# Performance work log

Hardware: AMD Instinct MI355X
Metric: run time of the kernel (lower is better)

Reference implementation:

```python
import jax, jax.numpy as jnp
import numpy as np


def _hat(w):
    # w [...,3] -> skew-symmetric [...,3,3]
    x, y, z = w[..., 0], w[..., 1], w[..., 2]
    o = jnp.zeros_like(x)
    return jnp.stack([
        jnp.stack([o, -z, y], -1),
        jnp.stack([z, o, -x], -1),
        jnp.stack([-y, x, o], -1)], -2)


def _expmap(twist):
    # SE(3) exponential map. twist [...,6] = (v, w); returns [...,4,4]
    v, w = twist[..., :3], twist[..., 3:]
    th = jnp.linalg.norm(w, axis=-1, keepdims=True)[..., None]  # [...,1,1]
    Wh = _hat(w)
    W2 = Wh @ Wh
    small = th < 1e-4
    safe = jnp.where(small, 1.0, th)
    A = jnp.where(small, 1.0 - th * th / 6.0, jnp.sin(safe) / safe)
    Bc = jnp.where(small, 0.5 - th * th / 24.0, (1.0 - jnp.cos(safe)) / (safe * safe))
    Cc = jnp.where(small, 1.0 / 6.0 - th * th / 120.0, (safe - jnp.sin(safe)) / (safe ** 3))
    I = jnp.eye(3, dtype=twist.dtype)
    R = I + A * Wh + Bc * W2
    V = I + Bc * Wh + Cc * W2
    t = (V @ v[..., None])[..., 0]
    top = jnp.concatenate([R, t[..., None]], -1)  # [...,3,4]
    bot = jnp.broadcast_to(jnp.array([0.0, 0.0, 0.0, 1.0], twist.dtype), top.shape[:-2] + (1, 4))
    return jnp.concatenate([top, bot], -2)


def setup_inputs() -> dict:
    key = jax.random.key(0)
    ks = jax.random.split(key, 5)
    B, C, H, W = 2, 16, 32, 32
    embeddings = 0.3 * jax.random.normal(ks[0], (B, C, H, W), jnp.float32)
    revisions = 0.1 * jax.random.normal(ks[1], (B, 3, H, W), jnp.float32)
    weights = jax.random.uniform(ks[2], (B, 3, H, W), jnp.float32, 0.1, 1.0)
    depth = jax.random.uniform(ks[3], (B, 1, H, W), jnp.float32, 1.0, 5.0)
    pix = (jnp.zeros((4, 4), jnp.float32)
           .at[0, 0].set(float(W)).at[1, 1].set(float(W))
           .at[0, 2].set(W / 2.0).at[1, 2].set(H / 2.0)
           .at[2, 2].set(1.0).at[3, 3].set(1.0))
    pix_T_camXs = jnp.tile(pix[None], (B, 1, 1))
    twists = 0.02 * jax.random.normal(ks[4], (B, H, W, 6), jnp.float32)
    Tmat = _expmap(twists)  # valid SE(3) per pixel [B,H,W,4,4]
    return dict(embeddings=embeddings, revisions=revisions, weights=weights,
                depth=depth, pix_T_camXs=pix_T_camXs, Tmat=Tmat)


def reference(embeddings, revisions, weights, depth, pix_T_camXs, Tmat):
    B, C, H, W = embeddings.shape
    N = H * W
    dt = embeddings.dtype

    # pairwise embedding affinity exp(-||e_i - e_k||_2)  [B,N,N]
    e = embeddings.reshape(B, C, N).transpose(0, 2, 1)  # [B,N,C]
    diff = e[:, :, None, :] - e[:, None, :, :]
    aff = jnp.exp(-jnp.linalg.norm(diff, axis=-1))

    fx, fy = pix_T_camXs[:, 0, 0], pix_T_camXs[:, 1, 1]
    x0, y0 = pix_T_camXs[:, 0, 2], pix_T_camXs[:, 1, 2]

    # depth -> pointcloud [B,N,3]
    ys, xs = jnp.meshgrid(jnp.arange(H, dtype=dt), jnp.arange(W, dtype=dt), indexing='ij')
    u, v = xs.reshape(-1), ys.reshape(-1)
    z = depth.reshape(B, N)
    X = (u[None] - x0[:, None]) * z / fx[:, None]
    Y = (v[None] - y0[:, None]) * z / fy[:, None]
    xyz = jnp.stack([X, Y, z], -1)

    T = Tmat.reshape(B, N, 4, 4)
    Rm, tv = T[..., :3, :3], T[..., :3, 3]
    # T_k applied to its own point, and T_i (anchor) applied to every point
    TjXj = jnp.einsum('bkpq,bkq->bkp', Rm, xyz) + tv                    # [B,N,3]
    TiXj = jnp.einsum('bipq,bkq->bikp', Rm, xyz) + tv[:, :, None, :]     # [B,Ni,Nk,3]

    def pie(P):
        # projection (u, v, 1/Z)
        sh = (B,) + (1,) * (P.ndim - 2)
        invz = 1.0 / P[..., 2]
        uu = fx.reshape(sh) * P[..., 0] * invz + x0.reshape(sh)
        vv = fy.reshape(sh) * P[..., 1] * invz + y0.reshape(sh)
        return jnp.stack([uu, vv, invz], -1)

    pie_TjXj = pie(TjXj)   # [B,N,3]
    pie_TiXj = pie(TiXj)   # [B,Ni,Nk,3]

    r = revisions.reshape(B, 3, N).transpose(0, 2, 1)                   # [B,N,3]
    residual = pie_TiXj - (pie_TjXj + r)[:, None]                       # [B,Ni,Nk,3]

    # projection Jacobian wrt 3D point, d = 1/Z of transformed point
    d = pie_TiXj[..., 2]
    Xp, Yp = TiXj[..., 0], TiXj[..., 1]
    sh = (B, 1, 1)
    fxr, fyr = fx.reshape(sh), fy.reshape(sh)
    z0 = jnp.zeros_like(d)
    Jp = jnp.stack([
        jnp.stack([fxr * d, z0, -fxr * Xp * d * d], -1),
        jnp.stack([z0, fyr * d, -fyr * Yp * d * d], -1),
        jnp.stack([z0, z0, -d * d], -1)], -2)                            # [B,Ni,Nk,3,3]

    # transformation Jacobian [I | hat(X)]  [B,Nk,3,6]
    I3 = jnp.broadcast_to(jnp.eye(3, dtype=dt), (B, N, 3, 3))
    JT = jnp.concatenate([I3, _hat(xyz)], -1)

    Jac = jnp.einsum('bikpq,bkqr->bikpr', Jp, JT)                        # [B,Ni,Nk,3,6]

    wflat = weights.reshape(B, 3, N).transpose(0, 2, 1)                  # [B,Nk,3]
    wts = aff[..., None] * wflat[:, None]                                # [B,Ni,Nk,3]

    WJ = wts[..., None] * Jac
    Hm = jnp.einsum('bikcp,bikcq->bipq', WJ, Jac)                        # [B,Ni,6,6]
    rhs = jnp.einsum('bikcp,bikc->bip', Jac, residual)                   # [B,Ni,6]

    delta = jnp.einsum('bipq,biq->bip', jnp.linalg.inv(Hm), rhs)         # [B,N,6]

    dT = _expmap(delta.reshape(B, H, W, 6))                              # [B,H,W,4,4]
    return dT @ Tmat
```

## Files before the change

kernel.cpp:

```cpp
#include <hip/hip_runtime.h>
#include <math.h>

#define BB 2
#define CC 16
#define HH 32
#define WW 32
#define NN (HH*WW)
#define NPX (BB*NN)
#define PH  512

__global__ __launch_bounds__(512, 2)
void dse3_mono3(const float* __restrict__ emb,
                const float* __restrict__ rev,
                const float* __restrict__ wgt,
                const float* __restrict__ dep,
                const float* __restrict__ pix,
                const float* __restrict__ Tm,
                float* __restrict__ out)
{
    __shared__ float4 sE0[PH], sE1[PH], sE2[PH], sE3[PH], sQ0[PH], sQ1[PH];
    __shared__ float2 sQ2[PH];

    int tid  = threadIdx.x;
    int lane = tid & 63;
    int wv   = tid >> 6;
    int px   = blockIdx.x * 8 + wv;
    int b    = px >> 10;
    int kpx  = px & (NN - 1);

    float fx = pix[b*16 + 0], fy = pix[b*16 + 5];
    float x0 = pix[b*16 + 2], y0 = pix[b*16 + 6];
    float ifx = __builtin_amdgcn_rcpf(fx);
    float ify = __builtin_amdgcn_rcpf(fy);

    float ei[16];
    float sei = 0.f;
    #pragma unroll
    for (int c = 0; c < 16; ++c) {
        ei[c] = emb[(size_t)b*CC*NN + (size_t)c*NN + kpx];
        sei += ei[c]*ei[c];
    }
    const float4* Tp4 = (const float4*)(Tm + (size_t)px * 16);
    float4 Tr0 = Tp4[0], Tr1 = Tp4[1], Tr2 = Tp4[2];

    float aM0=0.f, aM2=0.f, aM4=0.f, aM5=0.f, aM8=0.f;
    float aN0=0.f, aN1=0.f, aN2=0.f, aN3=0.f, aN4=0.f,
          aN5=0.f, aN6=0.f, aN7=0.f, aN8=0.f;
    float aP0=0.f, aP1=0.f, aP2=0.f, aP3=0.f, aP4=0.f, aP5=0.f;
    float aR0=0.f, aR1=0.f, aR2=0.f, aR3=0.f, aR4=0.f, aR5=0.f;

    #pragma unroll
    for (int phase = 0; phase < 2; ++phase) {
        {
            int r  = tid;
            int k  = phase*PH + r;
            int gk = b*NN + k;

            float se = 0.f;
            float ev[16];
            #pragma unroll
            for (int c = 0; c < 16; ++c) {
                ev[c] = emb[(size_t)b*CC*NN + (size_t)c*NN + k];
                se += ev[c]*ev[c];
            }
            float u = (float)(k & (WW - 1));
            float v = (float)((k & (NN-1)) >> 5);
            float z = dep[b*NN + k];
            float X = (u - x0) * z * ifx;
            float Y = (v - y0) * z * ify;

            const float4* T4 = (const float4*)(Tm + (size_t)gk * 16);
            float4 t0 = T4[0], t1 = T4[1], t2 = T4[2];
            float Tx = t0.x*X + t0.y*Y + t0.z*z + t0.w;
            float Ty = t1.x*X + t1.y*Y + t1.z*z + t1.w;
            float Tz = t2.x*X + t2.y*Y + t2.z*z + t2.w;
            float di = __builtin_amdgcn_rcpf(Tz);

            float p0 = fx*Tx*di + x0 + rev[(size_t)b*3*NN + 0*NN + k];
            float p1 = fy*Ty*di + y0 + rev[(size_t)b*3*NN + 1*NN + k];
            float p2 = di            + rev[(size_t)b*3*NN + 2*NN + k];
            float w0 = wgt[(size_t)b*3*NN + 0*NN + k];
            float w1 = wgt[(size_t)b*3*NN + 1*NN + k];
            float w2 = wgt[(size_t)b*3*NN + 2*NN + k];

            sE0[r] = make_float4(ev[0],  ev[1],  ev[2],  ev[3]);
            sE1[r] = make_float4(ev[4],  ev[5],  ev[6],  ev[7]);
            sE2[r] = make_float4(ev[8],  ev[9],  ev[10], ev[11]);
            sE3[r] = make_float4(ev[12], ev[13], ev[14], ev[15]);
            sQ0[r] = make_float4(X, Y, z, p0);
            sQ1[r] = make_float4(p1, p2, w0, w1);
            sQ2[r] = make_float2(w2, se);
        }
        __syncthreads();

        #pragma unroll 2
        for (int j = 0; j < 8; ++j) {
            int r = j*64 + lane;

            float4 k0 = sE0[r], k1 = sE1[r], k2 = sE2[r], k3 = sE3[r];
            float4 q0 = sQ0[r], q1 = sQ1[r];
            float2 q2 = sQ2[r];

            float d0 = k0.x*ei[0]  + k0.y*ei[1]  + k0.z*ei[2]  + k0.w*ei[3];
            float d1 = k1.x*ei[4]  + k1.y*ei[5]  + k1.z*ei[6]  + k1.w*ei[7];
            float d2 = k2.x*ei[8]  + k2.y*ei[9]  + k2.z*ei[10] + k2.w*ei[11];
            float d3 = k3.x*ei[12] + k3.y*ei[13] + k3.z*ei[14] + k3.w*ei[15];
            float dot = (d0 + d1) + (d2 + d3);
            float ssq = fmaxf(sei + q2.y - 2.f*dot, 0.f);
            float aff = __expf(-__builtin_amdgcn_sqrtf(ssq));

            float X = q0.x, Y = q0.y, Z = q0.z;
            float Tx = Tr0.x*X + Tr0.y*Y + Tr0.z*Z + Tr0.w;
            float Ty = Tr1.x*X + Tr1.y*Y + Tr1.z*Z + Tr1.w;
            float Tz = Tr2.x*X + Tr2.y*Y + Tr2.z*Z + Tr2.w;
            float di = __builtin_amdgcn_rcpf(Tz);

            float a =  fx*di;
            float e =  fy*di;
            float uu = a*Tx;
            float vv = e*Ty;
            float r0 = uu + x0 - q0.w;
            float r1 = vv + y0 - q1.x;
            float r2 = di      - q1.y;
            float c = -uu*di;
            float f = -vv*di;
            float g = -di*di;

            float y0v = a*r0;
            float y1v = e*r1;
            float y2v = c*r0 + f*r1 + g*r2;
            aR0 += y0v; aR1 += y1v; aR2 += y2v;
            aR3 += Z*y1v - Y*y2v;
            aR4 += X*y2v - Z*y0v;
            aR5 += Y*y0v - X*y1v;

            float w0 = aff*q1.z, w1 = aff*q1.w, w2 = aff*q2.x;
            float aw = w0*a, ew = w1*e;
            float m00 = aw*a, m02 = aw*c;
            float m11 = ew*e, m12 = ew*f;
            float m22 = w0*c*c + w1*f*f + w2*g*g;
            aM0 += m00; aM2 += m02; aM4 += m11; aM5 += m12; aM8 += m22;

            float n00 = -m02*Y;
            float n01 =  m02*X - m00*Z;
            float n02 =  m00*Y;
            float n10 =  m11*Z - m12*Y;
            float n11 =  m12*X;
            float n12 = -m11*X;
            float n20 =  m12*Z - m22*Y;
            float n21 =  m22*X - m02*Z;
            float n22 =  m02*Y - m12*X;
            aN0 += n00; aN1 += n01; aN2 += n02;
            aN3 += n10; aN4 += n11; aN5 += n12;
            aN6 += n20; aN7 += n21; aN8 += n22;

            aP0 += Z*n10 - Y*n20;
            aP1 += Z*n11 - Y*n21;
            aP2 += Z*n12 - Y*n22;
            aP3 += X*n21 - Z*n01;
            aP4 += X*n22 - Z*n02;
            aP5 += Y*n02 - X*n12;
        }
        __syncthreads();
    }

    float acc[26] = { aM0,aM2,aM4,aM5,aM8,
                      aN0,aN1,aN2,aN3,aN4,aN5,aN6,aN7,aN8,
                      aP0,aP1,aP2,aP3,aP4,aP5,
                      aR0,aR1,aR2,aR3,aR4,aR5 };
    #pragma unroll
    for (int off = 32; off > 0; off >>= 1)
        #pragma unroll
        for (int t = 0; t < 26; ++t)
            acc[t] += __shfl_xor(acc[t], off, 64);

    if (lane != 0) return;

    float am[6][6];
    am[0][0]=acc[0]; am[0][1]=0.f;    am[0][2]=acc[1];
    am[1][1]=acc[2]; am[1][2]=acc[3]; am[2][2]=acc[4];
    am[0][3]=acc[5];  am[0][4]=acc[6];  am[0][5]=acc[7];
    am[1][3]=acc[8];  am[1][4]=acc[9];  am[1][5]=acc[10];
    am[2][3]=acc[11]; am[2][4]=acc[12]; am[2][5]=acc[13];
    am[3][3]=acc[14]; am[3][4]=acc[15]; am[3][5]=acc[16];
    am[4][4]=acc[17]; am[4][5]=acc[18]; am[5][5]=acc[19];
    #pragma unroll
    for (int p = 0; p < 6; ++p)
        #pragma unroll
        for (int q = 0; q < p; ++q) am[p][q] = am[q][p];
    float rh[6] = { acc[20], acc[21], acc[22], acc[23], acc[24], acc[25] };

    float L[6][6], dinv[6];
    #pragma unroll
    for (int p = 0; p < 6; ++p) {
        #pragma unroll
        for (int q = 0; q <= p; ++q) {
            float sm = am[p][q];
            #pragma unroll
            for (int r = 0; r < q; ++r) sm -= L[p][r]*L[q][r];
            if (q == p) {
                float sq = __builtin_amdgcn_sqrtf(sm);
                L[p][p] = sq;
                dinv[p] = __builtin_amdgcn_rcpf(sq);
            } else {
                L[p][q] = sm * dinv[q];
            }
        }
    }
    float yv[6];
    #pragma unroll
    for (int p = 0; p < 6; ++p) {
        float sm = rh[p];
        #pragma unroll
        for (int r = 0; r < p; ++r) sm -= L[p][r]*yv[r];
        yv[p] = sm * dinv[p];
    }
    float sol[6];
    #pragma unroll
    for (int pi = 5; pi >= 0; --pi) {
        float sm = yv[pi];
        #pragma unroll
        for (int r = pi + 1; r < 6; ++r) sm -= L[r][pi]*sol[r];
        sol[pi] = sm * dinv[pi];
    }

    float vx = sol[0], vy = sol[1], vz = sol[2];
    float wx = sol[3], wy = sol[4], wz = sol[5];
    float th2 = wx*wx + wy*wy + wz*wz;
    float th  = __builtin_amdgcn_sqrtf(th2);
    float Ae, Be, Ce;
    if (th < 1e-4f) {
        Ae = 1.0f - th2*(1.0f/6.0f);
        Be = 0.5f - th2*(1.0f/24.0f);
        Ce = 1.0f/6.0f - th2*(1.0f/120.0f);
    } else {
        float sn = __sinf(th), cn = __cosf(th);
        float ith = __builtin_amdgcn_rcpf(th), ith2 = ith*ith;
        Ae = sn*ith;
        Be = (1.0f - cn)*ith2;
        Ce = (th - sn)*ith2*ith;
    }
    float Wh[3][3] = {{0.f,-wz, wy},{ wz,0.f,-wx},{-wy, wx,0.f}};
    float W2[3][3] = {{wx*wx - th2, wx*wy,       wx*wz      },
                      {wx*wy,       wy*wy - th2, wy*wz      },
                      {wx*wz,       wy*wz,       wz*wz - th2}};
    float Rd[3][3], Vd[3][3];
    #pragma unroll
    for (int p = 0; p < 3; ++p)
        #pragma unroll
        for (int q = 0; q < 3; ++q) {
            float idq = (p == q) ? 1.0f : 0.0f;
            Rd[p][q] = idq + Ae*Wh[p][q] + Be*W2[p][q];
            Vd[p][q] = idq + Be*Wh[p][q] + Ce*W2[p][q];
        }
    float td[3];
    #pragma unroll
    for (int p = 0; p < 3; ++p)
        td[p] = Vd[p][0]*vx + Vd[p][1]*vy + Vd[p][2]*vz;

    const float4 bot = Tp4[3];
    float* o = out + (size_t)px * 16;
    #pragma unroll
    for (int p = 0; p < 3; ++p) {
        float4 r;
        r.x = Rd[p][0]*Tr0.x + Rd[p][1]*Tr1.x + Rd[p][2]*Tr2.x + td[p]*bot.x;
        r.y = Rd[p][0]*Tr0.y + Rd[p][1]*Tr1.y + Rd[p][2]*Tr2.y + td[p]*bot.y;
        r.z = Rd[p][0]*Tr0.z + Rd[p][1]*Tr1.z + Rd[p][2]*Tr2.z + td[p]*bot.z;
        r.w = Rd[p][0]*Tr0.w + Rd[p][1]*Tr1.w + Rd[p][2]*Tr2.w + td[p]*bot.w;
        *(float4*)(o + p*4) = r;
    }
    *(float4*)(o + 12) = bot;
}

extern "C" void kernel_launch(void* const* d_in, const int* in_sizes, int n_in,
                              void* d_out, int out_size, void* d_ws, size_t ws_size,
                              hipStream_t stream) {
    const float* emb = (const float*)d_in[0];
    const float* rev = (const float*)d_in[1];
    const float* wgt = (const float*)d_in[2];
    const float* dep = (const float*)d_in[3];
    const float* pix = (const float*)d_in[4];
    const float* Tm  = (const float*)d_in[5];
    float* out = (float*)d_out;

    dse3_mono3<<<NPX/8, 512, 0, stream>>>(emb, rev, wgt, dep, pix, Tm, out);
}
```

Before: 22.77 us.

## Split each pixel's key loop across two waves with LDS partial-sum reduction

Doubles the block to 1024 threads so two waves share each output pixel, each covering half of every 512-key phase. Partial Hessian and RHS sums are reduced through shared memory before lane 0 of the even wave does the Cholesky solve. This shortens the serial per-wave inner loop and adds waves to hide latency. In exchange, half the threads sit idle during staging, there is an extra barrier and LDS round-trip, and dropping the occupancy hint may raise register pressure.

```diff
diff --git a/kernel.cpp b/kernel.cpp
--- a/kernel.cpp
+++ b/kernel.cpp
@@ -9,8 +9,8 @@
 #define NPX (BB*NN)
 #define PH  512
 
-__global__ __launch_bounds__(512, 2)
-void dse3_mono3(const float* __restrict__ emb,
+__global__ __launch_bounds__(1024)
+void dse3_mono4(const float* __restrict__ emb,
                 const float* __restrict__ rev,
                 const float* __restrict__ wgt,
                 const float* __restrict__ dep,
@@ -20,11 +20,14 @@
 {
     __shared__ float4 sE0[PH], sE1[PH], sE2[PH], sE3[PH], sQ0[PH], sQ1[PH];
     __shared__ float2 sQ2[PH];
+    __shared__ float  ldsR[16][26];
 
     int tid  = threadIdx.x;
     int lane = tid & 63;
     int wv   = tid >> 6;
-    int px   = blockIdx.x * 8 + wv;
+    int s    = wv >> 1;
+    int h    = wv & 1;
+    int px   = blockIdx.x * 8 + s;
     int b    = px >> 10;
     int kpx  = px & (NN - 1);
 
@@ -51,7 +54,7 @@
 
     #pragma unroll
     for (int phase = 0; phase < 2; ++phase) {
-        {
+        if (tid < PH) {
             int r  = tid;
             int k  = phase*PH + r;
             int gk = b*NN + k;
@@ -94,8 +97,8 @@
         __syncthreads();
 
         #pragma unroll 2
-        for (int j = 0; j < 8; ++j) {
-            int r = j*64 + lane;
+        for (int j = 0; j < 4; ++j) {
+            int r = h*256 + j*64 + lane;
 
             float4 k0 = sE0[r], k1 = sE1[r], k2 = sE2[r], k3 = sE3[r];
             float4 q0 = sQ0[r], q1 = sQ1[r];
@@ -174,21 +177,30 @@
         for (int t = 0; t < 26; ++t)
             acc[t] += __shfl_xor(acc[t], off, 64);
 
-    if (lane != 0) return;
+    if (lane == 0)
+        #pragma unroll
+        for (int t = 0; t < 26; ++t) ldsR[wv][t] = acc[t];
+    __syncthreads();
+
+    if (lane != 0 || (wv & 1)) return;
+
+    float hv[26];
+    #pragma unroll
+    for (int t = 0; t < 26; ++t) hv[t] = ldsR[wv][t] + ldsR[wv + 1][t];
 
     float am[6][6];
-    am[0][0]=acc[0]; am[0][1]=0.f;    am[0][2]=acc[1];
-    am[1][1]=acc[2]; am[1][2]=acc[3]; am[2][2]=acc[4];
-    am[0][3]=acc[5];  am[0][4]=acc[6];  am[0][5]=acc[7];
-    am[1][3]=acc[8];  am[1][4]=acc[9];  am[1][5]=acc[10];
-    am[2][3]=acc[11]; am[2][4]=acc[12]; am[2][5]=acc[13];
-    am[3][3]=acc[14]; am[3][4]=acc[15]; am[3][5]=acc[16];
-    am[4][4]=acc[17]; am[4][5]=acc[18]; am[5][5]=acc[19];
+    am[0][0]=hv[0]; am[0][1]=0.f;    am[0][2]=hv[1];
+    am[1][1]=hv[2]; am[1][2]=hv[3];  am[2][2]=hv[4];
+    am[0][3]=hv[5];  am[0][4]=hv[6];  am[0][5]=hv[7];
+    am[1][3]=hv[8];  am[1][4]=hv[9];  am[1][5]=hv[10];
+    am[2][3]=hv[11]; am[2][4]=hv[12]; am[2][5]=hv[13];
+    am[3][3]=hv[14]; am[3][4]=hv[15]; am[3][5]=hv[16];
+    am[4][4]=hv[17]; am[4][5]=hv[18]; am[5][5]=hv[19];
     #pragma unroll
     for (int p = 0; p < 6; ++p)
         #pragma unroll
         for (int q = 0; q < p; ++q) am[p][q] = am[q][p];
-    float rh[6] = { acc[20], acc[21], acc[22], acc[23], acc[24], acc[25] };
+    float rh[6] = { hv[20], hv[21], hv[22], hv[23], hv[24], hv[25] };
 
     float L[6][6], dinv[6];
     #pragma unroll
@@ -283,5 +295,5 @@
     const float* Tm  = (const float*)d_in[5];
     float* out = (float*)d_out;
 
-    dse3_mono3<<<NPX/8, 512, 0, stream>>>(emb, rev, wgt, dep, pix, Tm, out);
+    dse3_mono4<<<NPX/8, 1024, 0, stream>>>(emb, rev, wgt, dep, pix, Tm, out);
 }
```

Result: slower. 28.09 us (+23.3%).
